# Performance work log

Hardware: AMD Instinct MI355X
Metric: run time of the kernel (lower is better)

Reference implementation:

```python
import jax, jax.numpy as jnp
import numpy as np

N, B, T, C = 1024, 4, 12, 64
D, H, K, E = 64, 2, 3, 16384  # out_dim, gat heads, num_kernel, edges per kernel
NEG_SLOPE_ATTN = 0.2   # DGL GATConv default
NEG_SLOPE_ACT = 0.01   # nn.LeakyReLU default


def setup_inputs() -> dict:
    key = jax.random.key(0)
    ks = jax.random.split(key, 12)
    input_feature = jax.random.normal(ks[0], (B, N, T, C), dtype=jnp.float32)
    # edge lists per kernel, with self loops appended (dgl.add_self_loop)
    loops = jnp.broadcast_to(jnp.arange(N, dtype=jnp.int32), (K, N))
    src_idx = jnp.concatenate(
        [jax.random.randint(ks[1], (K, E), 0, N, dtype=jnp.int32), loops], axis=1)
    dst_idx = jnp.concatenate(
        [jax.random.randint(ks[2], (K, E), 0, N, dtype=jnp.int32), loops], axis=1)
    # GATConv params per kernel: fc (no bias), attn_l/attn_r, output bias
    fc_w = jax.random.normal(ks[3], (K, C, H * D), dtype=jnp.float32) * 0.1
    attn_l = jax.random.normal(ks[4], (K, H, D), dtype=jnp.float32) * 0.1
    attn_r = jax.random.normal(ks[5], (K, H, D), dtype=jnp.float32) * 0.1
    gat_bias = jax.random.normal(ks[6], (K, H * D), dtype=jnp.float32) * 0.02
    # per-kernel merge weight, init std 0.05 as in init_weight()
    weight = jax.random.normal(ks[7], (K,), dtype=jnp.float32) * 0.05
    # merge MLP: Linear(H*D -> D)
    merge_w = jax.random.normal(ks[8], (H * D, D), dtype=jnp.float32) * 0.05
    merge_b = jax.random.normal(ks[9], (D,), dtype=jnp.float32) * 0.02
    return {"input_feature": input_feature, "fc_w": fc_w, "attn_l": attn_l,
            "attn_r": attn_r, "gat_bias": gat_bias, "weight": weight,
            "merge_w": merge_w, "merge_b": merge_b,
            "src_idx": src_idx, "dst_idx": dst_idx}


def _gat_conv(x, fc_w, attn_l, attn_r, bias, src, dst):
    """DGL GATConv on feature x: [N,B,T,C] -> [N,B,T,H,D]."""
    feat = jnp.einsum('nbtc,ce->nbte', x, fc_w).reshape(N, B, T, H, D)
    el = jnp.einsum('nbthd,hd->nbth', feat, attn_l)  # [N,B,T,H]
    er = jnp.einsum('nbthd,hd->nbth', feat, attn_r)
    e = jax.nn.leaky_relu(el[src] + er[dst], NEG_SLOPE_ATTN)  # [Etot,B,T,H]
    # segment softmax over destination neighborhoods (self loops guarantee >=1 edge)
    emax = jax.ops.segment_max(e, dst, num_segments=N)
    a = jnp.exp(e - emax[dst])
    denom = jax.ops.segment_sum(a, dst, num_segments=N)
    alpha = a / denom[dst]
    msg = alpha[..., None] * feat[src]  # [Etot,B,T,H,D]
    rst = jax.ops.segment_sum(msg, dst, num_segments=N)
    return rst + bias.reshape(H, D)


def reference(input_feature, fc_w, attn_l, attn_r, gat_bias, weight,
              merge_w, merge_b, src_idx, dst_idx):
    x = jnp.transpose(input_feature, (1, 0, 2, 3))  # [N,B,T,C]
    result = jnp.zeros((N, B, T, H, D), dtype=x.dtype)
    for i in range(K):  # small fixed set of dilated kernels
        result = result + weight[i] * _gat_conv(
            x, fc_w[i], attn_l[i], attn_r[i], gat_bias[i], src_idx[i], dst_idx[i])
    merged = result.reshape(N, B, T, H * D) @ merge_w + merge_b  # [N,B,T,D]
    out = jax.nn.leaky_relu(merged, NEG_SLOPE_ACT) + x  # residual = Identity (C==D)
    return jnp.transpose(out, (1, 0, 2, 3))  # [B,N,T,D]
```

## Files before the change

### kernel.cpp

```cpp
#include <hip/hip_runtime.h>

#define NN   1024
#define TT   12
#define CC   64
#define DD   64
#define HH   2
#define KK   3
#define ETOT 17408
#define BT   48
#define BTH  96
#define HD   128
#define NODES (KK * NN + 1)
#define PADN  (KK * NN)
#define CSR_CAP (KK * ETOT + 12 * NN)
#define LOG2E 1.44269504f
#define MT   128
#define NBLK (NN * BT / MT)
#define EDGE_BLOCKS ((KK * ETOT + 255) / 256)

typedef __attribute__((ext_vector_type(8))) short s8v;
typedef __attribute__((ext_vector_type(4))) float f4v;

__device__ __forceinline__ float bf_lo(unsigned int u) {
    return __uint_as_float(u << 16);
}
__device__ __forceinline__ float bf_hi(unsigned int u) {
    return __uint_as_float(u & 0xFFFF0000u);
}
__device__ __forceinline__ unsigned short f2bf(float f) {
    unsigned int u = __float_as_uint(f);
    u += 0x7FFFu + ((u >> 16) & 1u);
    return (unsigned short)(u >> 16);
}
__device__ __forceinline__ unsigned int pack2(float a, float b) {
    return (unsigned int)f2bf(a) | ((unsigned int)f2bf(b) << 16);
}

__global__ __launch_bounds__(256) void aux_kernel(
    const int* __restrict__ dst_idx, int* __restrict__ counts,
    const float* __restrict__ fc_w, const float* __restrict__ attn_l,
    const float* __restrict__ attn_r, float* __restrict__ alc, float* __restrict__ arc,
    uint2* __restrict__ featp, float* __restrict__ elp)
{
    int bid = blockIdx.x;
    int t = threadIdx.x;
    if (bid < EDGE_BLOCKS) {
        int tid = bid * 256 + t;
        if (tid < KK * ETOT) {
            int k = tid / ETOT;
            atomicAdd(&counts[k * NN + dst_idx[tid]], 1);
        }
    } else {
        for (int item = t; item < KK * HH * CC; item += 256) {
            int kh = item >> 6, c = item & 63;
            int k = kh >> 1, h = kh & 1;
            float sl = 0.f, sr = 0.f;
            #pragma unroll
            for (int dd = 0; dd < 64; ++dd) {
                float wv = fc_w[k * CC * HD + c * HD + h * 64 + dd];
                sl = fmaf(wv, attn_l[k * HD + h * 64 + dd], sl);
                sr = fmaf(wv, attn_r[k * HD + h * 64 + dd], sr);
            }
            alc[item] = sl * LOG2E;
            arc[item] = sr * LOG2E;
        }
        for (int item = t; item < 24 * 64; item += 256)
            featp[((size_t)(item >> 6) * NODES + PADN) * 64 + (item & 63)] = make_uint2(0u, 0u);
        for (int item = t; item < 24 * 4; item += 256)
            elp[((size_t)(item >> 2) * NODES + PADN) * 4 + (item & 3)] = -1e30f;
    }
}

__global__ __launch_bounds__(256) void feat_mfma_kernel(
    const float* __restrict__ x,
    const float* __restrict__ fc_w,
    uint2* __restrict__ featp)
{
    int k  = blockIdx.x / NBLK;
    int m0 = (blockIdx.x - k * NBLK) * MT;
    int t  = threadIdx.x;
    int w  = t >> 6, l = t & 63;

    __shared__ __align__(16) unsigned short As[128 * 64];
    __shared__ __align__(16) unsigned short Ws[128 * 64];

    #pragma unroll
    for (int rep = 0; rep < 4; ++rep) {
        int gid = t + 256 * rep;
        int row = gid >> 3, g = gid & 7;
        int m = m0 + row;
        int n = m / BT, bt = m - n * BT;
        int b = bt / TT, tt2 = bt - b * TT;
        const float* xr = &x[(((size_t)b * NN + n) * TT + tt2) * CC + g * 8];
        float4 v0 = *(const float4*)xr;
        float4 v1 = *(const float4*)(xr + 4);
        uint4 pk = { pack2(v0.x, v0.y), pack2(v0.z, v0.w),
                     pack2(v1.x, v1.y), pack2(v1.z, v1.w) };
        *(uint4*)((char*)As + row * 128 + ((g ^ (row & 7)) << 4)) = pk;
    }
    #pragma unroll
    for (int rep = 0; rep < 4; ++rep) {
        int gid = t + 256 * rep;
        int e = gid & 127, g = gid >> 7;
        float v[8];
        #pragma unroll
        for (int jj = 0; jj < 8; ++jj)
            v[jj] = fc_w[(size_t)k * CC * HD + (g * 8 + jj) * HD + e];
        uint4 pk = { pack2(v[0], v[1]), pack2(v[2], v[3]),
                     pack2(v[4], v[5]), pack2(v[6], v[7]) };
        *(uint4*)((char*)Ws + e * 128 + ((g ^ (e & 7)) << 4)) = pk;
    }
    __syncthreads();

    int Mw = (w & 1) * 64;
    int Nw = (w >> 1) * 64;
    int rsel = l & 15, ksel = l >> 4;

    f4v acc[4][4];
    #pragma unroll
    for (int mi = 0; mi < 4; ++mi)
        #pragma unroll
        for (int nf = 0; nf < 4; ++nf)
            acc[mi][nf] = (f4v){0.f, 0.f, 0.f, 0.f};

    s8v af[4][2], bf[4][2];
    #pragma unroll
    for (int mi = 0; mi < 4; ++mi)
        #pragma unroll
        for (int ks = 0; ks < 2; ++ks) {
            int row = Mw + mi * 16 + rsel;
            int g = ks * 4 + ksel;
            af[mi][ks] = *(const s8v*)((const char*)As + row * 128 + ((g ^ (row & 7)) << 4));
        }
    #pragma unroll
    for (int nf = 0; nf < 4; ++nf)
        #pragma unroll
        for (int ks = 0; ks < 2; ++ks) {
            int e = Nw + nf * 16 + rsel;
            int g = ks * 4 + ksel;
            bf[nf][ks] = *(const s8v*)((const char*)Ws + e * 128 + ((g ^ (e & 7)) << 4));
        }

    #pragma unroll
    for (int mi = 0; mi < 4; ++mi)
        #pragma unroll
        for (int nf = 0; nf < 4; ++nf) {
            acc[mi][nf] = __builtin_amdgcn_mfma_f32_16x16x32_bf16(
                af[mi][0], bf[nf][0], acc[mi][nf], 0, 0, 0);
            acc[mi][nf] = __builtin_amdgcn_mfma_f32_16x16x32_bf16(
                af[mi][1], bf[nf][1], acc[mi][nf], 0, 0, 0);
        }

    int i0 = (l >> 4) * 4;
    #pragma unroll
    for (int mi = 0; mi < 4; ++mi) {
        int m = m0 + Mw + mi * 16 + i0;
        int n = m / BT, bt = m - n * BT;
        #pragma unroll
        for (int nf = 0; nf < 4; ++nf) {
            int e = Nw + nf * 16 + (l & 15);
            int h = e >> 6, d = e & 63;
            int s = (bt >> 2) * 2 + h;
            uint2 o = { pack2(acc[mi][nf][0], acc[mi][nf][1]),
                        pack2(acc[mi][nf][2], acc[mi][nf][3]) };
            featp[((size_t)s * NODES + k * NN + n) * 64 + d] = o;
        }
    }
}

__global__ __launch_bounds__(128) void elr_kernel(
    const float* __restrict__ x, const float* __restrict__ alc,
    const float* __restrict__ arc, float* __restrict__ elp, float* __restrict__ er)
{
    int n = blockIdx.x;
    int e = threadIdx.x;
    __shared__ float x_lds[BT * CC];
    __shared__ float cl[KK * HH * CC];
    __shared__ float cr[KK * HH * CC];

    for (int i = e; i < BT * CC; i += 128) {
        int bt = i >> 6, c = i & 63;
        int b = bt / TT, tt = bt - b * TT;
        x_lds[i] = x[(((size_t)b * NN + n) * TT + tt) * CC + c];
    }
    for (int i = e; i < KK * HH * CC; i += 128) { cl[i] = alc[i]; cr[i] = arc[i]; }
    __syncthreads();

    if (e < BTH) {
        int hh = e / BT, bt = e - hh * BT;
        #pragma unroll
        for (int k = 0; k < KK; ++k) {
            const float* alp = &cl[(k * HH + hh) * CC];
            const float* arp = &cr[(k * HH + hh) * CC];
            float sl = 0.f, sr = 0.f;
            #pragma unroll
            for (int cc = 0; cc < CC; ++cc) {
                int c = (cc + bt) & 63;
                float xv = x_lds[bt * CC + c];
                sl = fmaf(xv, alp[c], sl);
                sr = fmaf(xv, arp[c], sr);
            }
            int s = (bt >> 2) * 2 + hh;
            elp[((size_t)s * NODES + k * NN + n) * 4 + (bt & 3)] = sl;
            er[((size_t)(k * NN + n)) * BTH + e] = sr;
        }
    }
}

__global__ __launch_bounds__(1024) void scan_kernel(
    const int* __restrict__ counts,
    int4* __restrict__ segs, int* __restrict__ cursor, int* __restrict__ csr_comb)
{
    int n = threadIdx.x;
    int c0 = counts[n], c1 = counts[NN + n], c2 = counts[2 * NN + n];
    int p0 = (c0 + 3) & ~3, p1 = (c1 + 3) & ~3, p2 = (c2 + 3) & ~3;
    int tot = p0 + p1 + p2;
    __shared__ int buf[NN];
    buf[n] = tot;
    __syncthreads();
    for (int off = 1; off < NN; off <<= 1) {
        int v = (n >= off) ? buf[n - off] : 0;
        __syncthreads();
        buf[n] += v;
        __syncthreads();
    }
    int excl = buf[n] - tot;
    int4 sg;
    sg.x = excl; sg.y = excl + p0; sg.z = excl + p0 + p1; sg.w = excl + tot;
    segs[n] = sg;
    cursor[n] = sg.x;
    cursor[NN + n] = sg.y;
    cursor[2 * NN + n] = sg.z;
    for (int j = sg.x + c0; j < sg.y; ++j) csr_comb[j] = PADN;
    for (int j = sg.y + c1; j < sg.z; ++j) csr_comb[j] = PADN;
    for (int j = sg.z + c2; j < sg.w; ++j) csr_comb[j] = PADN;
}

__global__ void scatter_kernel(const int* __restrict__ src_idx,
                               const int* __restrict__ dst_idx,
                               int* __restrict__ cursor, int* __restrict__ csr_comb)
{
    int tid = blockIdx.x * blockDim.x + threadIdx.x;
    if (tid < KK * ETOT) {
        int k = tid / ETOT;
        int pos = atomicAdd(&cursor[k * NN + dst_idx[tid]], 1);
        csr_comb[pos] = k * NN + src_idx[tid];
    }
}

__global__ __launch_bounds__(256) void attn_kernel(
    const float* __restrict__ elp, const float* __restrict__ er,
    const int4* __restrict__ segs, const int* __restrict__ csr_comb,
    const float* __restrict__ weight, float* __restrict__ alpha)
{
    int bid = blockIdx.x;
    int xcd = bid & 7, q = bid >> 3;
    int sl = q / 64, nb = q - sl * 64;
    int s = xcd + 8 * sl;
    int w = threadIdx.x >> 6, l = threadIdx.x & 63;
    int btg4 = s >> 1, h = s & 1;
    int joff = l >> 2, bt = l & 3;
    const float* ep = elp + (size_t)s * NODES * 4;
    float* ap = alpha + (size_t)s * CSR_CAP * 4;

    for (int ni = 0; ni < 4; ++ni) {
        int n = nb * 16 + w * 4 + ni;
        int4 sg = segs[n];
        #pragma unroll
        for (int k = 0; k < KK; ++k) {
            int jb = (k == 0) ? sg.x : (k == 1) ? sg.y : sg.z;
            int je = (k == 0) ? sg.y : (k == 1) ? sg.z : sg.w;
            float erv = er[((size_t)(k * NN + n)) * BTH + h * BT + btg4 * 4 + bt];

            float ss = 0.f;
            for (int j0 = jb; j0 < je; j0 += 16) {
                int jj = j0 + joff;
                float a = 0.f;
                if (jj < je) {
                    int idx = csr_comb[jj];
                    float ev = ep[idx * 4 + bt] + erv;
                    ev = fmaxf(ev, ev * 0.2f);
                    a = __builtin_amdgcn_exp2f(ev);
                }
                ss += a;
            }
            #pragma unroll
            for (int off = 4; off < 64; off <<= 1)
                ss += __shfl_xor(ss, off, 64);
            float scale = weight[k] * __builtin_amdgcn_rcpf(ss);

            for (int j0 = jb; j0 < je; j0 += 16) {
                int jj = j0 + joff;
                if (jj < je) {
                    int idx = csr_comb[jj];
                    float ev = ep[idx * 4 + bt] + erv;
                    ev = fmaxf(ev, ev * 0.2f);
                    ap[(size_t)jj * 4 + bt] = __builtin_amdgcn_exp2f(ev) * scale;
                }
            }
        }
    }
}

__global__ __launch_bounds__(256) void agg_kernel(
    const uint2* __restrict__ featp,
    const float* __restrict__ alpha,
    const int4* __restrict__ segs, const int* __restrict__ csr_comb,
    const float* __restrict__ gat_bias, const float* __restrict__ weight,
    unsigned short* __restrict__ gatb)
{
    int j = ((int)blockIdx.x >> 3) + 768 * ((int)blockIdx.x & 7);
    int s = j >> 8;
    int g = j & 255;
    int w = threadIdx.x >> 6;
    int d = threadIdx.x & 63;
    int n = g * 4 + w;
    int btg4 = s >> 1, h = s & 1;
    int e = h * 64 + d;

    const uint2* fb = featp + (size_t)s * NODES * 64 + d;
    const float* ap = alpha + (size_t)s * CSR_CAP * 4;
    int4 sg = segs[n];
    int jb = __builtin_amdgcn_readfirstlane(sg.x);
    int je = __builtin_amdgcn_readfirstlane(sg.w);

    float r0 = 0.f, r1 = 0.f, r2 = 0.f, r3 = 0.f;

    #pragma unroll 2
    for (int jj = jb; jj < je; jj += 4) {
        int4 i4 = *(const int4*)&csr_comb[jj];
        int i0 = __builtin_amdgcn_readfirstlane(i4.x);
        int i1 = __builtin_amdgcn_readfirstlane(i4.y);
        int i2 = __builtin_amdgcn_readfirstlane(i4.z);
        int i3 = __builtin_amdgcn_readfirstlane(i4.w);
        uint2 f0 = fb[(size_t)i0 * 64];
        uint2 f1 = fb[(size_t)i1 * 64];
        uint2 f2 = fb[(size_t)i2 * 64];
        uint2 f3 = fb[(size_t)i3 * 64];
        float4 A0 = *(const float4*)&ap[(size_t)(jj + 0) * 4];
        float4 A1 = *(const float4*)&ap[(size_t)(jj + 1) * 4];
        float4 A2 = *(const float4*)&ap[(size_t)(jj + 2) * 4];
        float4 A3 = *(const float4*)&ap[(size_t)(jj + 3) * 4];

        r0 = fmaf(A0.x, bf_lo(f0.x), r0); r1 = fmaf(A0.y, bf_hi(f0.x), r1);
        r2 = fmaf(A0.z, bf_lo(f0.y), r2); r3 = fmaf(A0.w, bf_hi(f0.y), r3);

        r0 = fmaf(A1.x, bf_lo(f1.x), r0); r1 = fmaf(A1.y, bf_hi(f1.x), r1);
        r2 = fmaf(A1.z, bf_lo(f1.y), r2); r3 = fmaf(A1.w, bf_hi(f1.y), r3);

        r0 = fmaf(A2.x, bf_lo(f2.x), r0); r1 = fmaf(A2.y, bf_hi(f2.x), r1);
        r2 = fmaf(A2.z, bf_lo(f2.y), r2); r3 = fmaf(A2.w, bf_hi(f2.y), r3);

        r0 = fmaf(A3.x, bf_lo(f3.x), r0); r1 = fmaf(A3.y, bf_hi(f3.x), r1);
        r2 = fmaf(A3.z, bf_lo(f3.y), r2); r3 = fmaf(A3.w, bf_hi(f3.y), r3);
    }

    float wb = weight[0] * gat_bias[e] + weight[1] * gat_bias[HD + e]
             + weight[2] * gat_bias[2 * HD + e];
    r0 += wb; r1 += wb; r2 += wb; r3 += wb;

    size_t row = (size_t)n * BT + btg4 * 4;
    gatb[(row + 0) * HD + e] = f2bf(r0);
    gatb[(row + 1) * HD + e] = f2bf(r1);
    gatb[(row + 2) * HD + e] = f2bf(r2);
    gatb[(row + 3) * HD + e] = f2bf(r3);
}

__global__ __launch_bounds__(256) void merge_mfma_kernel(
    const unsigned short* __restrict__ gatb,
    const float* __restrict__ merge_w, const float* __restrict__ merge_b,
    const float* __restrict__ x, float* __restrict__ out)
{
    int m0 = blockIdx.x * 128;
    int t = threadIdx.x, w = t >> 6, l = t & 63;

    __shared__ __align__(16) unsigned short As[128 * 128];
    __shared__ __align__(16) unsigned short Bs[64 * 128];

    #pragma unroll
    for (int rep = 0; rep < 8; ++rep) {
        int gid = t + 256 * rep;
        int row = gid >> 4, gg = gid & 15;
        uint4 v = *(const uint4*)((const char*)gatb + ((size_t)(m0 + row)) * 256 + gg * 16);
        *(uint4*)((char*)As + row * 256 + ((gg ^ (row & 15)) << 4)) = v;
    }
    #pragma unroll
    for (int rep = 0; rep < 4; ++rep) {
        int gid = t + 256 * rep;
        int col = gid >> 4, gg = gid & 15;
        float v[8];
        #pragma unroll
        for (int jj = 0; jj < 8; ++jj)
            v[jj] = merge_w[(gg * 8 + jj) * DD + col];
        uint4 pk = { pack2(v[0], v[1]), pack2(v[2], v[3]),
                     pack2(v[4], v[5]), pack2(v[6], v[7]) };
        *(uint4*)((char*)Bs + col * 256 + ((gg ^ (col & 15)) << 4)) = pk;
    }
    __syncthreads();

    int Mw = (w & 1) * 64, Nw = (w >> 1) * 32;
    int rsel = l & 15, ksel = l >> 4;

    f4v acc[4][2];
    #pragma unroll
    for (int mi = 0; mi < 4; ++mi)
        #pragma unroll
        for (int nf = 0; nf < 2; ++nf)
            acc[mi][nf] = (f4v){0.f, 0.f, 0.f, 0.f};

    s8v af[4][4], bfr[2][4];
    #pragma unroll
    for (int mi = 0; mi < 4; ++mi)
        #pragma unroll
        for (int ks = 0; ks < 4; ++ks) {
            int row = Mw + mi * 16 + rsel;
            int g2 = ks * 4 + ksel;
            af[mi][ks] = *(const s8v*)((const char*)As + row * 256 + ((g2 ^ (row & 15)) << 4));
        }
    #pragma unroll
    for (int nf = 0; nf < 2; ++nf)
        #pragma unroll
        for (int ks = 0; ks < 4; ++ks) {
            int col = Nw + nf * 16 + rsel;
            int g2 = ks * 4 + ksel;
            bfr[nf][ks] = *(const s8v*)((const char*)Bs + col * 256 + ((g2 ^ (col & 15)) << 4));
        }

    #pragma unroll
    for (int mi = 0; mi < 4; ++mi)
        #pragma unroll
        for (int nf = 0; nf < 2; ++nf)
            #pragma unroll
            for (int ks = 0; ks < 4; ++ks)
                acc[mi][nf] = __builtin_amdgcn_mfma_f32_16x16x32_bf16(
                    af[mi][ks], bfr[nf][ks], acc[mi][nf], 0, 0, 0);

    int i0 = (l >> 4) * 4;
    #pragma unroll
    for (int mi = 0; mi < 4; ++mi) {
        int m = m0 + Mw + mi * 16 + i0;
        int n = m / BT, btb = m - n * BT;
        int b = btb / TT, t0 = btb - b * TT;
        #pragma unroll
        for (int nf = 0; nf < 2; ++nf) {
            int dd = Nw + nf * 16 + (l & 15);
            float mb = merge_b[dd];
            #pragma unroll
            for (int reg = 0; reg < 4; ++reg) {
                float mg = acc[mi][nf][reg] + mb;
                mg = mg > 0.f ? mg : mg * 0.01f;
                size_t oidx = (((size_t)b * NN + n) * TT + t0 + reg) * DD + dd;
                out[oidx] = mg + x[oidx];
            }
        }
    }
}

extern "C" void kernel_launch(void* const* d_in, const int* in_sizes, int n_in,
                              void* d_out, int out_size, void* d_ws, size_t ws_size,
                              hipStream_t stream)
{
    const float* x        = (const float*)d_in[0];
    const float* fc_w     = (const float*)d_in[1];
    const float* attn_l   = (const float*)d_in[2];
    const float* attn_r   = (const float*)d_in[3];
    const float* gat_bias = (const float*)d_in[4];
    const float* weight   = (const float*)d_in[5];
    const float* merge_w  = (const float*)d_in[6];
    const float* merge_b  = (const float*)d_in[7];
    const int*   src_idx  = (const int*)d_in[8];
    const int*   dst_idx  = (const int*)d_in[9];
    float*       out      = (float*)d_out;

    char* p = (char*)d_ws;
    auto carve = [&](size_t bytes) { char* r = p; p += (bytes + 15) & ~size_t(15); return r; };
    uint2* featp   = (uint2*)carve(sizeof(uint2) * (size_t)24 * NODES * 64);
    float* alpha   = (float*)carve(sizeof(float) * (size_t)24 * CSR_CAP * 4);
    unsigned short* gatb = (unsigned short*)carve(sizeof(unsigned short) * (size_t)NN * BT * HD);
    float* elp     = (float*)carve(sizeof(float) * (size_t)24 * NODES * 4);
    float* er      = (float*)carve(sizeof(float) * (size_t)KK * NN * BTH);
    float* alc     = (float*)carve(sizeof(float) * KK * HH * CC);
    float* arc     = (float*)carve(sizeof(float) * KK * HH * CC);
    int*   counts  = (int*)carve(sizeof(int) * KK * NN);
    int*   cursor  = (int*)carve(sizeof(int) * KK * NN);
    int4*  segs    = (int4*)carve(sizeof(int4) * NN);
    int*   csr_comb= (int*)carve(sizeof(int) * (CSR_CAP + 80));

    hipMemsetAsync(counts, 0, sizeof(int) * KK * NN, stream);

    aux_kernel<<<EDGE_BLOCKS + 1, 256, 0, stream>>>(
        dst_idx, counts, fc_w, attn_l, attn_r, alc, arc, featp, elp);

    feat_mfma_kernel<<<KK * NBLK, 256, 0, stream>>>(x, fc_w, featp);

    elr_kernel<<<NN, 128, 0, stream>>>(x, alc, arc, elp, er);

    scan_kernel<<<1, 1024, 0, stream>>>(counts, segs, cursor, csr_comb);
    scatter_kernel<<<EDGE_BLOCKS, 256, 0, stream>>>(src_idx, dst_idx, cursor, csr_comb);

    attn_kernel<<<1536, 256, 0, stream>>>(elp, er, segs, csr_comb, weight, alpha);

    agg_kernel<<<24 * 256, 256, 0, stream>>>(
        featp, alpha, segs, csr_comb, gat_bias, weight, gatb);

    merge_mfma_kernel<<<NN * BT / 128, 256, 0, stream>>>(gatb, merge_w, merge_b, x, out);
}
```

Baseline: 145.5 us.

## Fuse scatter, feature GEMM and el/er into one kernel; fold attention into aggregation

Three independent kernels (CSR scatter, bf16 MFMA feature projection, el/er dot products) are merged into one block-range-dispatched kernel, which saves launches and lets them run concurrently. The separate attention kernel and its global alpha buffer are removed. The aggregation kernel now computes the unnormalised exp scores per destination into LDS, reduces per-kernel sums, and applies normalisation and merge weights after the weighted feature sum. This removes a global write and read of alpha. The risks are that per-node in-degree must fit the fixed LDS capacity RUNCAP, and the aggregation kernel now holds more LDS and does more work per block.

New measurement: 145.4 us. About the same (-0.0%).

```diff
diff --git a/kernel.cpp b/kernel.cpp
--- a/kernel.cpp
+++ b/kernel.cpp
@@ -17,6 +17,9 @@
 #define MT   128
 #define NBLK (NN * BT / MT)
 #define EDGE_BLOCKS ((KK * ETOT + 255) / 256)
+#define FEAT_BLOCKS (KK * NBLK)
+#define BIG_BLOCKS (EDGE_BLOCKS + FEAT_BLOCKS + NN)
+#define RUNCAP 208
 
 typedef __attribute__((ext_vector_type(8))) short s8v;
 typedef __attribute__((ext_vector_type(4))) float f4v;
@@ -34,6 +37,9 @@
 }
 __device__ __forceinline__ unsigned int pack2(float a, float b) {
     return (unsigned int)f2bf(a) | ((unsigned int)f2bf(b) << 16);
+}
+__device__ __forceinline__ float rlf(float v, int lane) {
+    return __int_as_float(__builtin_amdgcn_readlane(__float_as_int(v), lane));
 }
 
 __global__ __launch_bounds__(256) void aux_kernel(
@@ -68,142 +74,6 @@
             featp[((size_t)(item >> 6) * NODES + PADN) * 64 + (item & 63)] = make_uint2(0u, 0u);
         for (int item = t; item < 24 * 4; item += 256)
             elp[((size_t)(item >> 2) * NODES + PADN) * 4 + (item & 3)] = -1e30f;
-    }
-}
-
-__global__ __launch_bounds__(256) void feat_mfma_kernel(
-    const float* __restrict__ x,
-    const float* __restrict__ fc_w,
-    uint2* __restrict__ featp)
-{
-    int k  = blockIdx.x / NBLK;
-    int m0 = (blockIdx.x - k * NBLK) * MT;
-    int t  = threadIdx.x;
-    int w  = t >> 6, l = t & 63;
-
-    __shared__ __align__(16) unsigned short As[128 * 64];
-    __shared__ __align__(16) unsigned short Ws[128 * 64];
-
-    #pragma unroll
-    for (int rep = 0; rep < 4; ++rep) {
-        int gid = t + 256 * rep;
-        int row = gid >> 3, g = gid & 7;
-        int m = m0 + row;
-        int n = m / BT, bt = m - n * BT;
-        int b = bt / TT, tt2 = bt - b * TT;
-        const float* xr = &x[(((size_t)b * NN + n) * TT + tt2) * CC + g * 8];
-        float4 v0 = *(const float4*)xr;
-        float4 v1 = *(const float4*)(xr + 4);
-        uint4 pk = { pack2(v0.x, v0.y), pack2(v0.z, v0.w),
-                     pack2(v1.x, v1.y), pack2(v1.z, v1.w) };
-        *(uint4*)((char*)As + row * 128 + ((g ^ (row & 7)) << 4)) = pk;
-    }
-    #pragma unroll
-    for (int rep = 0; rep < 4; ++rep) {
-        int gid = t + 256 * rep;
-        int e = gid & 127, g = gid >> 7;
-        float v[8];
-        #pragma unroll
-        for (int jj = 0; jj < 8; ++jj)
-            v[jj] = fc_w[(size_t)k * CC * HD + (g * 8 + jj) * HD + e];
-        uint4 pk = { pack2(v[0], v[1]), pack2(v[2], v[3]),
-                     pack2(v[4], v[5]), pack2(v[6], v[7]) };
-        *(uint4*)((char*)Ws + e * 128 + ((g ^ (e & 7)) << 4)) = pk;
-    }
-    __syncthreads();
-
-    int Mw = (w & 1) * 64;
-    int Nw = (w >> 1) * 64;
-    int rsel = l & 15, ksel = l >> 4;
-
-    f4v acc[4][4];
-    #pragma unroll
-    for (int mi = 0; mi < 4; ++mi)
-        #pragma unroll
-        for (int nf = 0; nf < 4; ++nf)
-            acc[mi][nf] = (f4v){0.f, 0.f, 0.f, 0.f};
-
-    s8v af[4][2], bf[4][2];
-    #pragma unroll
-    for (int mi = 0; mi < 4; ++mi)
-        #pragma unroll
-        for (int ks = 0; ks < 2; ++ks) {
-            int row = Mw + mi * 16 + rsel;
-            int g = ks * 4 + ksel;
-            af[mi][ks] = *(const s8v*)((const char*)As + row * 128 + ((g ^ (row & 7)) << 4));
-        }
-    #pragma unroll
-    for (int nf = 0; nf < 4; ++nf)
-        #pragma unroll
-        for (int ks = 0; ks < 2; ++ks) {
-            int e = Nw + nf * 16 + rsel;
-            int g = ks * 4 + ksel;
-            bf[nf][ks] = *(const s8v*)((const char*)Ws + e * 128 + ((g ^ (e & 7)) << 4));
-        }
-
-    #pragma unroll
-    for (int mi = 0; mi < 4; ++mi)
-        #pragma unroll
-        for (int nf = 0; nf < 4; ++nf) {
-            acc[mi][nf] = __builtin_amdgcn_mfma_f32_16x16x32_bf16(
-                af[mi][0], bf[nf][0], acc[mi][nf], 0, 0, 0);
-            acc[mi][nf] = __builtin_amdgcn_mfma_f32_16x16x32_bf16(
-                af[mi][1], bf[nf][1], acc[mi][nf], 0, 0, 0);
-        }
-
-    int i0 = (l >> 4) * 4;
-    #pragma unroll
-    for (int mi = 0; mi < 4; ++mi) {
-        int m = m0 + Mw + mi * 16 + i0;
-        int n = m / BT, bt = m - n * BT;
-        #pragma unroll
-        for (int nf = 0; nf < 4; ++nf) {
-            int e = Nw + nf * 16 + (l & 15);
-            int h = e >> 6, d = e & 63;
-            int s = (bt >> 2) * 2 + h;
-            uint2 o = { pack2(acc[mi][nf][0], acc[mi][nf][1]),
-                        pack2(acc[mi][nf][2], acc[mi][nf][3]) };
-            featp[((size_t)s * NODES + k * NN + n) * 64 + d] = o;
-        }
-    }
-}
-
-__global__ __launch_bounds__(128) void elr_kernel(
-    const float* __restrict__ x, const float* __restrict__ alc,
-    const float* __restrict__ arc, float* __restrict__ elp, float* __restrict__ er)
-{
-    int n = blockIdx.x;
-    int e = threadIdx.x;
-    __shared__ float x_lds[BT * CC];
-    __shared__ float cl[KK * HH * CC];
-    __shared__ float cr[KK * HH * CC];
-
-    for (int i = e; i < BT * CC; i += 128) {
-        int bt = i >> 6, c = i & 63;
-        int b = bt / TT, tt = bt - b * TT;
-        x_lds[i] = x[(((size_t)b * NN + n) * TT + tt) * CC + c];
-    }
-    for (int i = e; i < KK * HH * CC; i += 128) { cl[i] = alc[i]; cr[i] = arc[i]; }
-    __syncthreads();
-
-    if (e < BTH) {
-        int hh = e / BT, bt = e - hh * BT;
-        #pragma unroll
-        for (int k = 0; k < KK; ++k) {
-            const float* alp = &cl[(k * HH + hh) * CC];
-            const float* arp = &cr[(k * HH + hh) * CC];
-            float sl = 0.f, sr = 0.f;
-            #pragma unroll
-            for (int cc = 0; cc < CC; ++cc) {
-                int c = (cc + bt) & 63;
-                float xv = x_lds[bt * CC + c];
-                sl = fmaf(xv, alp[c], sl);
-                sr = fmaf(xv, arp[c], sr);
-            }
-            int s = (bt >> 2) * 2 + hh;
-            elp[((size_t)s * NODES + k * NN + n) * 4 + (bt & 3)] = sl;
-            er[((size_t)(k * NN + n)) * BTH + e] = sr;
-        }
     }
 }
 
@@ -236,75 +106,247 @@
     for (int j = sg.z + c2; j < sg.w; ++j) csr_comb[j] = PADN;
 }
 
-__global__ void scatter_kernel(const int* __restrict__ src_idx,
-                               const int* __restrict__ dst_idx,
-                               int* __restrict__ cursor, int* __restrict__ csr_comb)
+__global__ __launch_bounds__(256) void big_kernel(
+    const int* __restrict__ src_idx, const int* __restrict__ dst_idx,
+    int* __restrict__ cursor, int* __restrict__ csr_comb,
+    const float* __restrict__ x, const float* __restrict__ fc_w,
+    uint2* __restrict__ featp,
+    const float* __restrict__ alc, const float* __restrict__ arc,
+    float* __restrict__ elp, float* __restrict__ er)
 {
-    int tid = blockIdx.x * blockDim.x + threadIdx.x;
-    if (tid < KK * ETOT) {
-        int k = tid / ETOT;
-        int pos = atomicAdd(&cursor[k * NN + dst_idx[tid]], 1);
-        csr_comb[pos] = k * NN + src_idx[tid];
-    }
-}
-
-__global__ __launch_bounds__(256) void attn_kernel(
-    const float* __restrict__ elp, const float* __restrict__ er,
-    const int4* __restrict__ segs, const int* __restrict__ csr_comb,
-    const float* __restrict__ weight, float* __restrict__ alpha)
-{
+    __shared__ __align__(16) char smem[32768];
     int bid = blockIdx.x;
-    int xcd = bid & 7, q = bid >> 3;
-    int sl = q / 64, nb = q - sl * 64;
-    int s = xcd + 8 * sl;
-    int w = threadIdx.x >> 6, l = threadIdx.x & 63;
-    int btg4 = s >> 1, h = s & 1;
-    int joff = l >> 2, bt = l & 3;
-    const float* ep = elp + (size_t)s * NODES * 4;
-    float* ap = alpha + (size_t)s * CSR_CAP * 4;
-
-    for (int ni = 0; ni < 4; ++ni) {
-        int n = nb * 16 + w * 4 + ni;
-        int4 sg = segs[n];
-        #pragma unroll
-        for (int k = 0; k < KK; ++k) {
-            int jb = (k == 0) ? sg.x : (k == 1) ? sg.y : sg.z;
-            int je = (k == 0) ? sg.y : (k == 1) ? sg.z : sg.w;
-            float erv = er[((size_t)(k * NN + n)) * BTH + h * BT + btg4 * 4 + bt];
-
-            float ss = 0.f;
-            for (int j0 = jb; j0 < je; j0 += 16) {
-                int jj = j0 + joff;
-                float a = 0.f;
-                if (jj < je) {
-                    int idx = csr_comb[jj];
-                    float ev = ep[idx * 4 + bt] + erv;
-                    ev = fmaxf(ev, ev * 0.2f);
-                    a = __builtin_amdgcn_exp2f(ev);
+    int t = threadIdx.x;
+
+    if (bid < EDGE_BLOCKS) {
+        int tid = bid * 256 + t;
+        if (tid < KK * ETOT) {
+            int k = tid / ETOT;
+            int pos = atomicAdd(&cursor[k * NN + dst_idx[tid]], 1);
+            csr_comb[pos] = k * NN + src_idx[tid];
+        }
+        return;
+    }
+    if (bid < EDGE_BLOCKS + FEAT_BLOCKS) {
+        int kb = bid - EDGE_BLOCKS;
+        int k  = kb / NBLK;
+        int m0 = (kb - k * NBLK) * MT;
+        int w  = t >> 6, l = t & 63;
+        unsigned short* As = (unsigned short*)smem;
+        unsigned short* Ws = (unsigned short*)(smem + 16384);
+
+        #pragma unroll
+        for (int rep = 0; rep < 4; ++rep) {
+            int gid = t + 256 * rep;
+            int row = gid >> 3, g = gid & 7;
+            int m = m0 + row;
+            int n = m / BT, bt = m - n * BT;
+            int b = bt / TT, tt2 = bt - b * TT;
+            const float* xr = &x[(((size_t)b * NN + n) * TT + tt2) * CC + g * 8];
+            float4 v0 = *(const float4*)xr;
+            float4 v1 = *(const float4*)(xr + 4);
+            uint4 pk = { pack2(v0.x, v0.y), pack2(v0.z, v0.w),
+                         pack2(v1.x, v1.y), pack2(v1.z, v1.w) };
+            *(uint4*)((char*)As + row * 128 + ((g ^ (row & 7)) << 4)) = pk;
+        }
+        #pragma unroll
+        for (int rep = 0; rep < 4; ++rep) {
+            int gid = t + 256 * rep;
+            int e = gid & 127, g = gid >> 7;
+            float v[8];
+            #pragma unroll
+            for (int jj = 0; jj < 8; ++jj)
+                v[jj] = fc_w[(size_t)k * CC * HD + (g * 8 + jj) * HD + e];
+            uint4 pk = { pack2(v[0], v[1]), pack2(v[2], v[3]),
+                         pack2(v[4], v[5]), pack2(v[6], v[7]) };
+            *(uint4*)((char*)Ws + e * 128 + ((g ^ (e & 7)) << 4)) = pk;
+        }
+        __syncthreads();
+
+        int Mw = (w & 1) * 64;
+        int Nw = (w >> 1) * 64;
+        int rsel = l & 15, ksel = l >> 4;
+
+        f4v acc[4][4];
+        #pragma unroll
+        for (int mi = 0; mi < 4; ++mi)
+            #pragma unroll
+            for (int nf = 0; nf < 4; ++nf)
+                acc[mi][nf] = (f4v){0.f, 0.f, 0.f, 0.f};
+
+        s8v af[4][2], bf[4][2];
+        #pragma unroll
+        for (int mi = 0; mi < 4; ++mi)
+            #pragma unroll
+            for (int ks = 0; ks < 2; ++ks) {
+                int row = Mw + mi * 16 + rsel;
+                int g = ks * 4 + ksel;
+                af[mi][ks] = *(const s8v*)((const char*)As + row * 128 + ((g ^ (row & 7)) << 4));
+            }
+        #pragma unroll
+        for (int nf = 0; nf < 4; ++nf)
+            #pragma unroll
+            for (int ks = 0; ks < 2; ++ks) {
+                int e = Nw + nf * 16 + rsel;
+                int g = ks * 4 + ksel;
+                bf[nf][ks] = *(const s8v*)((const char*)Ws + e * 128 + ((g ^ (e & 7)) << 4));
+            }
+
+        #pragma unroll
+        for (int mi = 0; mi < 4; ++mi)
+            #pragma unroll
+            for (int nf = 0; nf < 4; ++nf) {
+                acc[mi][nf] = __builtin_amdgcn_mfma_f32_16x16x32_bf16(
+                    af[mi][0], bf[nf][0], acc[mi][nf], 0, 0, 0);
+                acc[mi][nf] = __builtin_amdgcn_mfma_f32_16x16x32_bf16(
+                    af[mi][1], bf[nf][1], acc[mi][nf], 0, 0, 0);
+            }
+
+        int i0 = (l >> 4) * 4;
+        #pragma unroll
+        for (int mi = 0; mi < 4; ++mi) {
+            int m = m0 + Mw + mi * 16 + i0;
+            int n = m / BT, bt = m - n * BT;
+            #pragma unroll
+            for (int nf = 0; nf < 4; ++nf) {
+                int e = Nw + nf * 16 + (l & 15);
+                int h = e >> 6, d = e & 63;
+                int s = (bt >> 2) * 2 + h;
+                uint2 o = { pack2(acc[mi][nf][0], acc[mi][nf][1]),
+                            pack2(acc[mi][nf][2], acc[mi][nf][3]) };
+                featp[((size_t)s * NODES + k * NN + n) * 64 + d] = o;
+            }
+        }
+        return;
+    }
+
+    {
+        int n = bid - (EDGE_BLOCKS + FEAT_BLOCKS);
+        float* x_lds = (float*)smem;
+        float* cl    = (float*)(smem + 12288);
+        float* cr    = (float*)(smem + 12288 + 1536);
+
+        for (int i = t; i < BT * CC; i += 256) {
+            int bt = i >> 6, c = i & 63;
+            int b = bt / TT, tt = bt - b * TT;
+            x_lds[i] = x[(((size_t)b * NN + n) * TT + tt) * CC + c];
+        }
+        for (int i = t; i < KK * HH * CC; i += 256) { cl[i] = alc[i]; cr[i] = arc[i]; }
+        __syncthreads();
+
+        if (t < BTH) {
+            int hh = t / BT, bt = t - hh * BT;
+            #pragma unroll
+            for (int k = 0; k < KK; ++k) {
+                const float* alp = &cl[(k * HH + hh) * CC];
+                const float* arp = &cr[(k * HH + hh) * CC];
+                float sl = 0.f, sr = 0.f;
+                #pragma unroll
+                for (int cc = 0; cc < CC; ++cc) {
+                    int c = (cc + bt) & 63;
+                    float xv = x_lds[bt * CC + c];
+                    sl = fmaf(xv, alp[c], sl);
+                    sr = fmaf(xv, arp[c], sr);
                 }
-                ss += a;
-            }
-            #pragma unroll
-            for (int off = 4; off < 64; off <<= 1)
-                ss += __shfl_xor(ss, off, 64);
-            float scale = weight[k] * __builtin_amdgcn_rcpf(ss);
-
-            for (int j0 = jb; j0 < je; j0 += 16) {
-                int jj = j0 + joff;
-                if (jj < je) {
-                    int idx = csr_comb[jj];
-                    float ev = ep[idx * 4 + bt] + erv;
-                    ev = fmaxf(ev, ev * 0.2f);
-                    ap[(size_t)jj * 4 + bt] = __builtin_amdgcn_exp2f(ev) * scale;
-                }
-            }
-        }
-    }
-}
+                int s = (bt >> 2) * 2 + hh;
+                elp[((size_t)s * NODES + k * NN + n) * 4 + (bt & 3)] = sl;
+                er[((size_t)(k * NN + n)) * BTH + t] = sr;
+            }
+        }
+    }
+}
+
+#define EDGE_FMA8(F, A)                                        \
+    r0 = fmaf((A).x, bf_lo((F).x), r0);                        \
+    r1 = fmaf((A).y, bf_hi((F).x), r1);                        \
+    r2 = fmaf((A).z, bf_lo((F).y), r2);                        \
+    r3 = fmaf((A).w, bf_hi((F).y), r3);
+
+#define PHASE1(JB, JE, KIDX, SC4) {                                            \
+    int jb = (JB), je = (JE);                                                  \
+    float erv = er[((size_t)((KIDX) * NN + n)) * BTH + h * BT + btg4 * 4 + bt];\
+    float ss = 0.f;                                                            \
+    for (int j0 = jb; j0 < je; j0 += 16) {                                     \
+        int jj = j0 + joff;                                                    \
+        float a = 0.f;                                                         \
+        if (jj < je) {                                                         \
+            int idx = csr_comb[jj];                                            \
+            float ev = ep[idx * 4 + bt] + erv;                                 \
+            ev = fmaxf(ev, ev * 0.2f);                                         \
+            a = __builtin_amdgcn_exp2f(ev);                                    \
+            alds[w][jj - base0][bt] = a;                                       \
+        }                                                                      \
+        ss += a;                                                               \
+    }                                                                          \
+    _Pragma("unroll")                                                          \
+    for (int off = 4; off < 64; off <<= 1) ss += __shfl_xor(ss, off, 64);      \
+    float wk_ = weight[KIDX];                                                  \
+    SC4 = make_float4(wk_ * __builtin_amdgcn_rcpf(rlf(ss, 0)),                 \
+                      wk_ * __builtin_amdgcn_rcpf(rlf(ss, 1)),                 \
+                      wk_ * __builtin_amdgcn_rcpf(rlf(ss, 2)),                 \
+                      wk_ * __builtin_amdgcn_rcpf(rlf(ss, 3))); }
+
+#define PHASE2(JB, JE, SC4) {                                                  \
+    int jb = __builtin_amdgcn_readfirstlane(JB);                               \
+    int je = __builtin_amdgcn_readfirstlane(JE);                               \
+    float r0 = 0.f, r1 = 0.f, r2 = 0.f, r3 = 0.f;                              \
+    int jj = jb;                                                               \
+    for (; jj + 8 <= je; jj += 8) {                                            \
+        int4 ia = *(const int4*)&csr_comb[jj];                                 \
+        int4 ib = *(const int4*)&csr_comb[jj + 4];                             \
+        int i0 = __builtin_amdgcn_readfirstlane(ia.x);                         \
+        int i1 = __builtin_amdgcn_readfirstlane(ia.y);                         \
+        int i2 = __builtin_amdgcn_readfirstlane(ia.z);                         \
+        int i3 = __builtin_amdgcn_readfirstlane(ia.w);                         \
+        int i4 = __builtin_amdgcn_readfirstlane(ib.x);                         \
+        int i5 = __builtin_amdgcn_readfirstlane(ib.y);                         \
+        int i6 = __builtin_amdgcn_readfirstlane(ib.z);                         \
+        int i7 = __builtin_amdgcn_readfirstlane(ib.w);                         \
+        uint2 f0 = fb[(size_t)i0 * 64];                                        \
+        uint2 f1 = fb[(size_t)i1 * 64];                                        \
+        uint2 f2 = fb[(size_t)i2 * 64];                                        \
+        uint2 f3 = fb[(size_t)i3 * 64];                                        \
+        uint2 f4 = fb[(size_t)i4 * 64];                                        \
+        uint2 f5 = fb[(size_t)i5 * 64];                                        \
+        uint2 f6 = fb[(size_t)i6 * 64];                                        \
+        uint2 f7 = fb[(size_t)i7 * 64];                                        \
+        float4 A0 = *(const float4*)&alds[w][jj - base0 + 0][0];               \
+        float4 A1 = *(const float4*)&alds[w][jj - base0 + 1][0];               \
+        float4 A2 = *(const float4*)&alds[w][jj - base0 + 2][0];               \
+        float4 A3 = *(const float4*)&alds[w][jj - base0 + 3][0];               \
+        float4 A4 = *(const float4*)&alds[w][jj - base0 + 4][0];               \
+        float4 A5 = *(const float4*)&alds[w][jj - base0 + 5][0];               \
+        float4 A6 = *(const float4*)&alds[w][jj - base0 + 6][0];               \
+        float4 A7 = *(const float4*)&alds[w][jj - base0 + 7][0];               \
+        EDGE_FMA8(f0, A0); EDGE_FMA8(f1, A1);                                  \
+        EDGE_FMA8(f2, A2); EDGE_FMA8(f3, A3);                                  \
+        EDGE_FMA8(f4, A4); EDGE_FMA8(f5, A5);                                  \
+        EDGE_FMA8(f6, A6); EDGE_FMA8(f7, A7);                                  \
+    }                                                                          \
+    if (jj < je) {                                                             \
+        int4 ia = *(const int4*)&csr_comb[jj];                                 \
+        int i0 = __builtin_amdgcn_readfirstlane(ia.x);                         \
+        int i1 = __builtin_amdgcn_readfirstlane(ia.y);                         \
+        int i2 = __builtin_amdgcn_readfirstlane(ia.z);                         \
+        int i3 = __builtin_amdgcn_readfirstlane(ia.w);                         \
+        uint2 f0 = fb[(size_t)i0 * 64];                                        \
+        uint2 f1 = fb[(size_t)i1 * 64];                                        \
+        uint2 f2 = fb[(size_t)i2 * 64];                                        \
+        uint2 f3 = fb[(size_t)i3 * 64];                                        \
+        float4 A0 = *(const float4*)&alds[w][jj - base0 + 0][0];               \
+        float4 A1 = *(const float4*)&alds[w][jj - base0 + 1][0];               \
+        float4 A2 = *(const float4*)&alds[w][jj - base0 + 2][0];               \
+        float4 A3 = *(const float4*)&alds[w][jj - base0 + 3][0];               \
+        EDGE_FMA8(f0, A0); EDGE_FMA8(f1, A1);                                  \
+        EDGE_FMA8(f2, A2); EDGE_FMA8(f3, A3);                                  \
+    }                                                                          \
+    acc0 = fmaf(r0, (SC4).x, acc0); acc1 = fmaf(r1, (SC4).y, acc1);            \
+    acc2 = fmaf(r2, (SC4).z, acc2); acc3 = fmaf(r3, (SC4).w, acc3); }
 
 __global__ __launch_bounds__(256) void agg_kernel(
     const uint2* __restrict__ featp,
-    const float* __restrict__ alpha,
+    const float* __restrict__ elp,
+    const float* __restrict__ er,
     const int4* __restrict__ segs, const int* __restrict__ csr_comb,
     const float* __restrict__ gat_bias, const float* __restrict__ weight,
     unsigned short* __restrict__ gatb)
@@ -313,58 +355,42 @@
     int s = j >> 8;
     int g = j & 255;
     int w = threadIdx.x >> 6;
-    int d = threadIdx.x & 63;
+    int l = threadIdx.x & 63;
     int n = g * 4 + w;
     int btg4 = s >> 1, h = s & 1;
-    int e = h * 64 + d;
-
-    const uint2* fb = featp + (size_t)s * NODES * 64 + d;
-    const float* ap = alpha + (size_t)s * CSR_CAP * 4;
+    int e = h * 64 + l;
+
+    __shared__ __align__(16) float alds[4][RUNCAP][4];
+
+    const uint2* fb = featp + (size_t)s * NODES * 64 + l;
+    const float* ep = elp + (size_t)s * NODES * 4;
     int4 sg = segs[n];
-    int jb = __builtin_amdgcn_readfirstlane(sg.x);
-    int je = __builtin_amdgcn_readfirstlane(sg.w);
-
-    float r0 = 0.f, r1 = 0.f, r2 = 0.f, r3 = 0.f;
-
-    #pragma unroll 2
-    for (int jj = jb; jj < je; jj += 4) {
-        int4 i4 = *(const int4*)&csr_comb[jj];
-        int i0 = __builtin_amdgcn_readfirstlane(i4.x);
-        int i1 = __builtin_amdgcn_readfirstlane(i4.y);
-        int i2 = __builtin_amdgcn_readfirstlane(i4.z);
-        int i3 = __builtin_amdgcn_readfirstlane(i4.w);
-        uint2 f0 = fb[(size_t)i0 * 64];
-        uint2 f1 = fb[(size_t)i1 * 64];
-        uint2 f2 = fb[(size_t)i2 * 64];
-        uint2 f3 = fb[(size_t)i3 * 64];
-        float4 A0 = *(const float4*)&ap[(size_t)(jj + 0) * 4];
-        float4 A1 = *(const float4*)&ap[(size_t)(jj + 1) * 4];
-        float4 A2 = *(const float4*)&ap[(size_t)(jj + 2) * 4];
-        float4 A3 = *(const float4*)&ap[(size_t)(jj + 3) * 4];
-
-        r0 = fmaf(A0.x, bf_lo(f0.x), r0); r1 = fmaf(A0.y, bf_hi(f0.x), r1);
-        r2 = fmaf(A0.z, bf_lo(f0.y), r2); r3 = fmaf(A0.w, bf_hi(f0.y), r3);
-
-        r0 = fmaf(A1.x, bf_lo(f1.x), r0); r1 = fmaf(A1.y, bf_hi(f1.x), r1);
-        r2 = fmaf(A1.z, bf_lo(f1.y), r2); r3 = fmaf(A1.w, bf_hi(f1.y), r3);
-
-        r0 = fmaf(A2.x, bf_lo(f2.x), r0); r1 = fmaf(A2.y, bf_hi(f2.x), r1);
-        r2 = fmaf(A2.z, bf_lo(f2.y), r2); r3 = fmaf(A2.w, bf_hi(f2.y), r3);
-
-        r0 = fmaf(A3.x, bf_lo(f3.x), r0); r1 = fmaf(A3.y, bf_hi(f3.x), r1);
-        r2 = fmaf(A3.z, bf_lo(f3.y), r2); r3 = fmaf(A3.w, bf_hi(f3.y), r3);
-    }
+    int base0 = __builtin_amdgcn_readfirstlane(sg.x);
+
+    int joff = l >> 2, bt = l & 3;
+    float4 sc0, sc1, sc2;
+    PHASE1(sg.x, sg.y, 0, sc0)
+    PHASE1(sg.y, sg.z, 1, sc1)
+    PHASE1(sg.z, sg.w, 2, sc2)
+
+    float acc0 = 0.f, acc1 = 0.f, acc2 = 0.f, acc3 = 0.f;
+    PHASE2(sg.x, sg.y, sc0)
+    PHASE2(sg.y, sg.z, sc1)
+    PHASE2(sg.z, sg.w, sc2)
 
     float wb = weight[0] * gat_bias[e] + weight[1] * gat_bias[HD + e]
              + weight[2] * gat_bias[2 * HD + e];
-    r0 += wb; r1 += wb; r2 += wb; r3 += wb;
+    acc0 += wb; acc1 += wb; acc2 += wb; acc3 += wb;
 
     size_t row = (size_t)n * BT + btg4 * 4;
-    gatb[(row + 0) * HD + e] = f2bf(r0);
-    gatb[(row + 1) * HD + e] = f2bf(r1);
-    gatb[(row + 2) * HD + e] = f2bf(r2);
-    gatb[(row + 3) * HD + e] = f2bf(r3);
-}
+    gatb[(row + 0) * HD + e] = f2bf(acc0);
+    gatb[(row + 1) * HD + e] = f2bf(acc1);
+    gatb[(row + 2) * HD + e] = f2bf(acc2);
+    gatb[(row + 3) * HD + e] = f2bf(acc3);
+}
+#undef EDGE_FMA8
+#undef PHASE1
+#undef PHASE2
 
 __global__ __launch_bounds__(256) void merge_mfma_kernel(
     const unsigned short* __restrict__ gatb,
@@ -475,7 +501,6 @@
     char* p = (char*)d_ws;
     auto carve = [&](size_t bytes) { char* r = p; p += (bytes + 15) & ~size_t(15); return r; };
     uint2* featp   = (uint2*)carve(sizeof(uint2) * (size_t)24 * NODES * 64);
-    float* alpha   = (float*)carve(sizeof(float) * (size_t)24 * CSR_CAP * 4);
     unsigned short* gatb = (unsigned short*)carve(sizeof(unsigned short) * (size_t)NN * BT * HD);
     float* elp     = (float*)carve(sizeof(float) * (size_t)24 * NODES * 4);
     float* er      = (float*)carve(sizeof(float) * (size_t)KK * NN * BTH);
@@ -491,17 +516,13 @@
     aux_kernel<<<EDGE_BLOCKS + 1, 256, 0, stream>>>(
         dst_idx, counts, fc_w, attn_l, attn_r, alc, arc, featp, elp);
 
-    feat_mfma_kernel<<<KK * NBLK, 256, 0, stream>>>(x, fc_w, featp);
-
-    elr_kernel<<<NN, 128, 0, stream>>>(x, alc, arc, elp, er);
-
     scan_kernel<<<1, 1024, 0, stream>>>(counts, segs, cursor, csr_comb);
-    scatter_kernel<<<EDGE_BLOCKS, 256, 0, stream>>>(src_idx, dst_idx, cursor, csr_comb);
-
-    attn_kernel<<<1536, 256, 0, stream>>>(elp, er, segs, csr_comb, weight, alpha);
+
+    big_kernel<<<BIG_BLOCKS, 256, 0, stream>>>(
+        src_idx, dst_idx, cursor, csr_comb, x, fc_w, featp, alc, arc, elp, er);
 
     agg_kernel<<<24 * 256, 256, 0, stream>>>(
-        featp, alpha, segs, csr_comb, gat_bias, weight, gatb);
+        featp, elp, er, segs, csr_comb, gat_bias, weight, gatb);
 
     merge_mfma_kernel<<<NN * BT / 128, 256, 0, stream>>>(gatb, merge_w, merge_b, x, out);
 }
```
